# Kernel optimization log

Measured on AMD Instinct MI355X. Metric: run time of the kernel, lower is better.

## Reference

```python
import jax, jax.numpy as jnp
import numpy as np

B, T, L = 64, 1024, 400
E, D, A, K = 512, 80, 512, 5  # enc_odim, dec_odim, attn_dim, num mixture components


def setup_inputs() -> dict:
    key = jax.random.key(0)
    ks = jax.random.split(key, 24)
    g = lambda k, shape, fan: jax.random.normal(k, shape, jnp.float32) / np.sqrt(fan)
    return {
        "enc_z": jax.random.normal(ks[0], (B, T, E), jnp.float32),
        "ys": jax.random.normal(ks[1], (B, L, D), jnp.float32),
        "pre_W1": g(ks[2], (D, D), D), "pre_b1": jnp.zeros((D,), jnp.float32),
        "pre_W2": g(ks[3], (D, D), D), "pre_b2": jnp.zeros((D,), jnp.float32),
        # MOL attention GRU cell: input D -> hidden A (gates r,z,n)
        "gru_Wx": g(ks[4], (D, 3 * A), D), "gru_Wh": g(ks[5], (A, 3 * A), A),
        "gru_bx": jnp.zeros((3 * A,), jnp.float32), "gru_bh": jnp.zeros((3 * A,), jnp.float32),
        # MOL param net: Linear(A,A) + tanh + Linear(A, 3K)
        "att_W1": g(ks[6], (A, A), A), "att_b1": jnp.zeros((A,), jnp.float32),
        "att_W2": g(ks[7], (A, 3 * K), A), "att_b2": jnp.zeros((3 * K,), jnp.float32),
        # 2-layer LSTM: layer1 input E+A -> D, layer2 D -> D (gates i,f,g,o)
        "lstm_Wx1": g(ks[8], (E + A, 4 * D), E + A), "lstm_Wh1": g(ks[9], (D, 4 * D), D),
        "lstm_b1": jnp.zeros((4 * D,), jnp.float32),
        "lstm_Wx2": g(ks[10], (D, 4 * D), D), "lstm_Wh2": g(ks[11], (D, 4 * D), D),
        "lstm_b2": jnp.zeros((4 * D,), jnp.float32),
        # stop token projection
        "stop_W": g(ks[12], (D, 1), D), "stop_b": jnp.zeros((1,), jnp.float32),
    }


def _gru_cell(x, h, Wx, Wh, bx, bh):
    gx = x @ Wx + bx
    gh = h @ Wh + bh
    xr, xz, xn = jnp.split(gx, 3, axis=-1)
    hr, hz, hn = jnp.split(gh, 3, axis=-1)
    r = jax.nn.sigmoid(xr + hr)
    z = jax.nn.sigmoid(xz + hz)
    n = jnp.tanh(xn + r * hn)
    return (1.0 - z) * n + z * h


def _lstm_cell(x, h, c, Wx, Wh, b):
    gates = x @ Wx + h @ Wh + b
    i, f, g_, o = jnp.split(gates, 4, axis=-1)
    c_new = jax.nn.sigmoid(f) * c + jax.nn.sigmoid(i) * jnp.tanh(g_)
    h_new = jax.nn.sigmoid(o) * jnp.tanh(c_new)
    return h_new, c_new


def reference(enc_z, ys, pre_W1, pre_b1, pre_W2, pre_b2,
              gru_Wx, gru_Wh, gru_bx, gru_bh,
              att_W1, att_b1, att_W2, att_b2,
              lstm_Wx1, lstm_Wh1, lstm_b1, lstm_Wx2, lstm_Wh2, lstm_b2,
              stop_W, stop_b):
    b, t, e = enc_z.shape
    n_steps = ys.shape[1]
    d = pre_W1.shape[0]
    a = gru_Wh.shape[0]
    k = att_W2.shape[1] // 3
    pos = jnp.arange(t, dtype=jnp.float32)  # encoder positions

    def step(carry, _):
        h_att, means, h1, c1, h2, c2, prev_out = carry
        # prenet (eval mode)
        p = jax.nn.relu(prev_out @ pre_W1 + pre_b1)
        p = jax.nn.relu(p @ pre_W2 + pre_b2)
        # MOL attention: update attention RNN state, predict mixture params
        h_att = _gru_cell(p, h_att, gru_Wx, gru_Wh, gru_bx, gru_bh)
        params = jnp.tanh(h_att @ att_W1 + att_b1) @ att_W2 + att_b2  # [B, 3K]
        mu_hat, s_hat, w_hat = jnp.split(params, 3, axis=-1)
        means = means + jax.nn.softplus(mu_hat)            # monotonic means [B, K]
        scales = jax.nn.softplus(s_hat) + 1e-4             # [B, K]
        mix_w = jax.nn.softmax(w_hat, axis=-1)             # [B, K]
        # attention weights via logistic CDF differences: [B, T, K] -> [B, T]
        z_hi = (pos[None, :, None] + 0.5 - means[:, None, :]) / scales[:, None, :]
        z_lo = (pos[None, :, None] - 0.5 - means[:, None, :]) / scales[:, None, :]
        attn_w = jnp.einsum('btk,bk->bt', jax.nn.sigmoid(z_hi) - jax.nn.sigmoid(z_lo), mix_w)
        context = jnp.einsum('bt,bte->be', attn_w, enc_z)  # [B, E]
        # 2-layer LSTM
        x = jnp.concatenate([context, h_att], axis=-1)     # [B, E+A]
        h1, c1 = _lstm_cell(x, h1, c1, lstm_Wx1, lstm_Wh1, lstm_b1)
        h2, c2 = _lstm_cell(h1, h2, c2, lstm_Wx2, lstm_Wh2, lstm_b2)
        logit = (h2 @ stop_W + stop_b)[:, 0]               # [B]
        new_carry = (h_att, means, h1, c1, h2, c2, h2)     # feedback = decoder output
        return new_carry, (h2, logit)

    zf = lambda *s: jnp.zeros(s, jnp.float32)
    carry0 = (zf(b, a), zf(b, k), zf(b, d), zf(b, d), zf(b, d), zf(b, d), zf(b, d))
    _, (outs, logits) = jax.lax.scan(step, carry0, xs=None, length=n_steps)
    before = jnp.transpose(outs, (1, 0, 2))   # [B, L, D]
    after = before                             # postnet not applied inside loop
    return after, before, jnp.transpose(logits, (1, 0))  # [B, L]
```

## Files before the change

### kernel.cpp

```cpp
#include <hip/hip_runtime.h>

#define NB 256
#define BT 512
#define BB 64
#define TT 1024
#define LL 400
#define EE 512
#define DD 80
#define AA 512
#define KK 5

#define WF_HB 2048
#define WF_PP 34816
#define WF_PL 51200
#define WF_EW 112640
#define WF_EWSZ (64UL*1024UL*320UL)

struct Pr {
  const float *enc;
  const float *pW1,*pb1,*pW2,*pb2;
  const float *gWx,*gWh,*gbx,*gbh;
  const float *aW1,*ab1,*aW2,*ab2;
  const float *lWx1,*lWh1,*lb1,*lWx2,*lWh2,*lb2;
  const float *sW,*sb;
  float *oa,*obf,*ol;
  unsigned *ctr;
  float *hb,*pp,*pls,*ew;
  int useEW;
};

__device__ __forceinline__ float sigm(float x){ return 1.f/(1.f+expf(-x)); }
__device__ __forceinline__ float softplusf(float x){ return fmaxf(x,0.f)+log1pf(expf(-fabsf(x))); }
__device__ __forceinline__ void gstore(float* p, float v){
  __hip_atomic_store(p, v, __ATOMIC_RELAXED, __HIP_MEMORY_SCOPE_AGENT);
}
__device__ __forceinline__ float gload(const float* p){
  return __hip_atomic_load(p, __ATOMIC_RELAXED, __HIP_MEMORY_SCOPE_AGENT);
}
__device__ __forceinline__ void gadd(float* p, float v){
  __hip_atomic_fetch_add(p, v, __ATOMIC_RELAXED, __HIP_MEMORY_SCOPE_AGENT);
}
__device__ __forceinline__ void acc4(float4& a, float w, const float4 x){
  a.x = fmaf(w,x.x,a.x); a.y = fmaf(w,x.y,a.y);
  a.z = fmaf(w,x.z,a.z); a.w = fmaf(w,x.w,a.w);
}

__device__ __forceinline__ void cbar_arrive(unsigned* ctr){
  __syncthreads();
  if (threadIdx.x == 0){
    asm volatile("s_waitcnt vmcnt(0)" ::: "memory");
    __hip_atomic_fetch_add(ctr, 1u, __ATOMIC_RELAXED, __HIP_MEMORY_SCOPE_AGENT);
  }
}
__device__ __forceinline__ void cbar_wait(unsigned* ctr, unsigned& tgt){
  if (threadIdx.x == 0){
    while (__hip_atomic_load(ctr, __ATOMIC_RELAXED, __HIP_MEMORY_SCOPE_AGENT) < tgt)
      __builtin_amdgcn_s_sleep(1);
  }
  __syncthreads();
  tgt += 16;
}

__global__ __launch_bounds__(512) void ew_kernel(const float* __restrict__ enc,
                                                 const float* __restrict__ W,
                                                 float* __restrict__ EW){
  const int b = blockIdx.x, t0 = blockIdx.y*16, tid = threadIdx.x;
  __shared__ float encT[512*16];
  #pragma unroll
  for (int r=0;r<16;++r)
    encT[tid*16+r] = enc[((size_t)b*TT + t0 + r)*EE + tid];
  __syncthreads();
  if (tid < 320){
    float acc[16];
    #pragma unroll
    for (int k=0;k<16;++k) acc[k]=0.f;
    const float* wp = W + tid;
    #pragma unroll 2
    for (int e=0;e<512;++e){
      float w = wp[(size_t)e*320];
      const float4* er = (const float4*)&encT[e*16];
      float4 x0=er[0], x1=er[1], x2=er[2], x3=er[3];
      acc[0]=fmaf(w,x0.x,acc[0]); acc[1]=fmaf(w,x0.y,acc[1]);
      acc[2]=fmaf(w,x0.z,acc[2]); acc[3]=fmaf(w,x0.w,acc[3]);
      acc[4]=fmaf(w,x1.x,acc[4]); acc[5]=fmaf(w,x1.y,acc[5]);
      acc[6]=fmaf(w,x1.z,acc[6]); acc[7]=fmaf(w,x1.w,acc[7]);
      acc[8]=fmaf(w,x2.x,acc[8]); acc[9]=fmaf(w,x2.y,acc[9]);
      acc[10]=fmaf(w,x2.z,acc[10]); acc[11]=fmaf(w,x2.w,acc[11]);
      acc[12]=fmaf(w,x3.x,acc[12]); acc[13]=fmaf(w,x3.y,acc[13]);
      acc[14]=fmaf(w,x3.z,acc[14]); acc[15]=fmaf(w,x3.w,acc[15]);
    }
    #pragma unroll
    for (int k=0;k<16;++k)
      EW[((size_t)b*TT + t0 + k)*320 + tid] = acc[k];
  }
}

__global__ __launch_bounds__(BT) void decoder_kernel(Pr P){
  const int blk = blockIdx.x, tid = threadIdx.x;
  const int sq = blk & 15, coh = blk >> 4;
  const int b0 = coh * 4;
  unsigned* ctr = P.ctr + coh*64;

  __shared__ float4 hj4[512];
  __shared__ float4 pj4[DD];
  __shared__ float4 h1j4[DD];
  __shared__ float4 h2j4[DD];
  __shared__ float4 qs4[32];
  __shared__ float4 ctx4[32];
  __shared__ float4 l2a4[320];
  __shared__ float4 scr4[2048];
  __shared__ float  awb[4][1024];
  __shared__ float  c1s[4][80], c2s[4][80];
  __shared__ float  pv[4][16], msta[4][8], mscl[4][8], mwt[4][8];
  __shared__ float  stp[320];
  __shared__ int    wlo[4], whi[4];

  float* hjF=(float*)hj4;  float* pjF=(float*)pj4;  float* h1F=(float*)h1j4;
  float* h2F=(float*)h2j4; float* scrF=(float*)scr4; float* qsF=(float*)qs4;

  { float4 z{};
    for (int i=tid;i<512;i+=BT) hj4[i]=z;
    for (int i=tid;i<1536;i+=BT) scr4[512+i]=z;
    if (tid<DD){ h1j4[tid]=z; h2j4[tid]=z; }
    if (tid<320){ c1s[tid&3][tid>>2]=0.f; c2s[tid&3][tid>>2]=0.f; }
    if (tid<32) msta[tid>>3][tid&7]=0.f;
  }
  if (tid<320){
    #pragma unroll
    for (int par=0;par<3;++par)
      #pragma unroll
      for (int g=0;g<4;++g)
        gstore(&P.pls[par*20480 + (size_t)(b0+g)*320 + tid], 0.f);
  }
  unsigned tgt = 16;
  cbar_arrive(ctr); cbar_wait(ctr, tgt);

  for (int l=0; l<LL; ++l){
    float* plA = P.pls + (l%3)*20480;
    float* plZ = P.pls + ((l+1)%3)*20480;

    if (tid<320){
      const int col=tid>>2, g=tid&3;
      float s=P.pb1[col];
      #pragma unroll 4
      for (int j=0;j<DD;++j) s = fmaf(h2F[j*4+g], P.pW1[j*DD+col], s);
      scrF[col*4+g]=fmaxf(s,0.f);
    }
    __syncthreads();
    if (tid<320){
      const int col=tid>>2, g=tid&3;
      float s=P.pb2[col];
      #pragma unroll 4
      for (int j=0;j<DD;++j) s = fmaf(scrF[j*4+g], P.pW2[j*DD+col], s);
      pjF[col*4+g]=fmaxf(s,0.f);
    }
    __syncthreads();

    if (tid<128){
      const int u = tid & 31, psl = tid >> 5;
      const int cb = sq*32 + u;
      float4 ar{}, az{}, axn{};
      const int j0 = psl*20;
      #pragma unroll 4
      for (int jj=0;jj<20;++jj){
        const int j = j0+jj;
        float4 x = pj4[j];
        const float* W = P.gWx + (size_t)j*1536 + cb;
        acc4(ar,W[0],x); acc4(az,W[512],x); acc4(axn,W[1024],x);
      }
      scr4[0*128 + psl*32+u]=ar;
      scr4[1*128 + psl*32+u]=az;
      scr4[2*128 + psl*32+u]=axn;
    }
    __syncthreads();
    if (tid<128){
      const int u=tid>>2, g=tid&3, uu=sq*32+u;
      float rx=0,zx=0,xn=0,hn=0;
      #pragma unroll
      for (int k=0;k<4;++k){
        rx += scrF[(0*128+k*32+u)*4+g];
        zx += scrF[(1*128+k*32+u)*4+g];
        xn += scrF[(2*128+k*32+u)*4+g];
      }
      #pragma unroll
      for (int k=0;k<16;++k){
        rx += scrF[(512 + 0*512 + k*32+u)*4+g];
        zx += scrF[(512 + 1*512 + k*32+u)*4+g];
        hn += scrF[(512 + 2*512 + k*32+u)*4+g];
      }
      float r = sigm(rx + P.gbx[uu] + P.gbh[uu]);
      float z = sigm(zx + P.gbx[512+uu] + P.gbh[512+uu]);
      float n = tanhf(xn + P.gbx[1024+uu] + r*(hn + P.gbh[1024+uu]));
      float ho = (1.f-z)*n + z*hjF[uu*4+g];
      gstore(&P.hb[(size_t)(b0+g)*512 + uu], ho);
    }
    cbar_arrive(ctr);
    if (tid<320){
      float4 a{};
      const float* W = P.lWh2 + tid;
      #pragma unroll 4
      for (int j=0;j<DD;++j) acc4(a, W[(size_t)j*320], h2j4[j]);
      l2a4[tid]=a;
    }
    cbar_wait(ctr, tgt);
    {
      float4 h;
      h.x=gload(&P.hb[(size_t)(b0+0)*512+tid]);
      h.y=gload(&P.hb[(size_t)(b0+1)*512+tid]);
      h.z=gload(&P.hb[(size_t)(b0+2)*512+tid]);
      h.w=gload(&P.hb[(size_t)(b0+3)*512+tid]);
      hj4[tid]=h;
    }
    __syncthreads();

    {
      const int c = tid & 31, jsl = tid >> 5, j0 = jsl*32;
      float4 a{};
      const float* W = P.aW1 + (size_t)j0*512 + sq*32 + c;
      #pragma unroll 4
      for (int jj=0;jj<32;++jj) acc4(a, W[(size_t)jj*512], hj4[j0+jj]);
      scr4[jsl*32+c]=a;
    }
    __syncthreads();
    if (tid<128){
      const int c=tid>>2, g=tid&3;
      float s=0.f;
      #pragma unroll
      for (int k=0;k<16;++k) s += scrF[(k*32+c)*4+g];
      qsF[c*4+g] = tanhf(s + P.ab1[sq*32+c]);
    }
    __syncthreads();
    if (tid<60){
      const int col=tid%15, g=tid/15;
      float s=0.f;
      #pragma unroll 4
      for (int j=0;j<32;++j) s = fmaf(qsF[j*4+g], P.aW2[(size_t)(sq*32+j)*15+col], s);
      gstore(&P.pp[(size_t)(b0+g)*256 + sq*16 + col], s);
    }
    cbar_arrive(ctr);
    float4 l1acc{};
    if (tid<320){
      { const float* W = P.lWx1 + (size_t)(512+sq*32)*320 + tid;
        #pragma unroll 4
        for (int j=0;j<32;++j) acc4(l1acc, W[(size_t)j*320], hj4[sq*32+j]); }
      { const float* W = P.lWh1 + (size_t)(sq*5)*320 + tid;
        #pragma unroll
        for (int j=0;j<5;++j)  acc4(l1acc, W[(size_t)j*320], h1j4[sq*5+j]); }
    }
    cbar_wait(ctr, tgt);
    if (tid<60){
      const int col=tid%15, g=tid/15;
      float s=P.ab2[col];
      #pragma unroll
      for (int k=0;k<16;++k) s += gload(&P.pp[(size_t)(b0+g)*256 + k*16 + col]);
      pv[g][col]=s;
    }
    __syncthreads();
    if (tid<4){
      const int g=tid;
      float lo=3.4e38f, hi=-3.4e38f, mmax=-3.4e38f;
      #pragma unroll
      for (int k=0;k<KK;++k){
        float m = msta[g][k] + softplusf(pv[g][k]);
        msta[g][k]=m;
        float sc = softplusf(pv[g][5+k]) + 1e-4f;
        mscl[g][k]=sc;
        mmax = fmaxf(mmax, pv[g][10+k]);
        lo = fminf(lo, m-0.5f-26.f*sc);
        hi = fmaxf(hi, m+0.5f+26.f*sc);
      }
      float den=0.f;
      #pragma unroll
      for (int k=0;k<KK;++k){ float e=expf(pv[g][10+k]-mmax); mwt[g][k]=e; den+=e; }
      float rd=1.f/den;
      #pragma unroll
      for (int k=0;k<KK;++k) mwt[g][k]*=rd;
      int ilo=(int)fmaxf(0.f,floorf(lo));
      int ihi=(int)fminf((float)TT,ceilf(hi)+1.f);
      if (ihi<ilo) ihi=ilo;
      wlo[g]=ilo; whi[g]=ihi;
    }
    __syncthreads();

    if (P.useEW){
      { const int g = tid>>7, lane = tid&127;
        const int lo_=wlo[g], hi_=whi[g];
        for (int t = lo_+lane; t < hi_; t += 128){
          const float tf=(float)t;
          float s=0.f;
          #pragma unroll
          for (int k=0;k<KK;++k){
            float mu=msta[g][k], sc=mscl[g][k];
            s += mwt[g][k]*(sigm((tf+0.5f-mu)/sc)-sigm((tf-0.5f-mu)/sc));
          }
          awb[g][t-lo_]=s;
        }
      }
      __syncthreads();
      if (tid<320){
        float* lp=(float*)&l1acc;
        const float* EWb = P.ew;
        #pragma unroll
        for (int g=0;g<4;++g){
          const int lo_=wlo[g], hi_=whi[g];
          for (int t=lo_+sq; t<hi_; t+=16)
            lp[g] = fmaf(awb[g][t-lo_], EWb[((size_t)(b0+g)*TT+t)*320+tid], lp[g]);
        }
      }
    } else {
      { const int eq = tid&7, g = (tid>>3)&3, ts = tid>>5;
        const float* bz = P.enc + (size_t)(b0+g)*TT*EE + sq*32 + eq*4;
        float4 acc{};
        for (int t = wlo[g]+ts; t < whi[g]; t += 16){
          const float tf=(float)t;
          float awv=0.f;
          #pragma unroll
          for (int k=0;k<KK;++k){
            float mu=msta[g][k], sc=mscl[g][k];
            awv += mwt[g][k]*(sigm((tf+0.5f-mu)/sc)-sigm((tf-0.5f-mu)/sc));
          }
          float4 v = *(const float4*)(bz+(size_t)t*EE);
          acc.x=fmaf(awv,v.x,acc.x); acc.y=fmaf(awv,v.y,acc.y);
          acc.z=fmaf(awv,v.z,acc.z); acc.w=fmaf(awv,v.w,acc.w);
        }
        ((float4*)scrF)[ts*32 + g*8 + eq]=acc;
      }
      __syncthreads();
      if (tid<128){
        const int g=tid>>5, e=tid&31;
        float s=0.f;
        #pragma unroll
        for (int k=0;k<16;++k) s += scrF[(k*32 + g*8 + (e>>2))*4 + (e&3)];
        ((float*)&ctx4[e])[g]=s;
      }
      __syncthreads();
      if (tid<320){
        const float* W = P.lWx1 + (size_t)(sq*32)*320 + tid;
        #pragma unroll 4
        for (int j=0;j<32;++j) acc4(l1acc, W[(size_t)j*320], ctx4[j]);
      }
    }
    if (tid<320){
      float* lp=(float*)&l1acc;
      #pragma unroll
      for (int g=0;g<4;++g) gadd(&plA[(size_t)(b0+g)*320 + tid], lp[g]);
    }
    cbar_arrive(ctr);
    {
      const int u = tid & 31, hsl = tid >> 5;
      const int cb = sq*32 + u;
      float4 ar{}, az{}, ahn{};
      const int h0 = hsl*32;
      #pragma unroll 4
      for (int jj=0;jj<32;++jj){
        float4 x = hj4[h0+jj];
        const float* W = P.gWh + (size_t)(h0+jj)*1536 + cb;
        acc4(ar,W[0],x); acc4(az,W[512],x); acc4(ahn,W[1024],x);
      }
      scr4[512 + 0*512 + hsl*32+u]=ar;
      scr4[512 + 1*512 + hsl*32+u]=az;
      scr4[512 + 2*512 + hsl*32+u]=ahn;
    }
    cbar_wait(ctr, tgt);
    if (tid<320){
      const int u=tid>>2, g=tid&3;
      float gate[4];
      #pragma unroll
      for (int gg=0;gg<4;++gg)
        gate[gg] = gload(&plA[(size_t)(b0+g)*320 + gg*80 + u]) + P.lb1[gg*80+u];
      float i_=sigm(gate[0]), f_=sigm(gate[1]), g_=tanhf(gate[2]), o_=sigm(gate[3]);
      float cn=f_*c1s[g][u]+i_*g_;
      c1s[g][u]=cn;
      h1F[u*4+g]=o_*tanhf(cn);
    }
    if (sq==0 && tid<320){
      #pragma unroll
      for (int g=0;g<4;++g) gstore(&plZ[(size_t)(b0+g)*320 + tid], 0.f);
    }
    __syncthreads();
    if (tid<320){
      float4 a = l2a4[tid];
      const float* W = P.lWx2 + tid;
      #pragma unroll 4
      for (int j=0;j<DD;++j) acc4(a, W[(size_t)j*320], h1j4[j]);
      const float bb=P.lb2[tid];
      a.x+=bb; a.y+=bb; a.z+=bb; a.w+=bb;
      scr4[tid]=a;
    }
    __syncthreads();
    if (tid<320){
      const int u=tid>>2, g=tid&3;
      float i_=sigm(scrF[(0*80+u)*4+g]);
      float f_=sigm(scrF[(1*80+u)*4+g]);
      float g_=tanhf(scrF[(2*80+u)*4+g]);
      float o_=sigm(scrF[(3*80+u)*4+g]);
      float cn=f_*c2s[g][u]+i_*g_;
      c2s[g][u]=cn;
      float hn=o_*tanhf(cn);
      h2F[u*4+g]=hn;
      stp[u*4+g]=hn*P.sW[u];
      if (sq==0){
        const size_t o=((size_t)(b0+g)*LL+l)*DD+u;
        P.oa[o]=hn; P.obf[o]=hn;
      }
    }
    __syncthreads();
    if (tid<4 && sq==0){
      float s=P.sb[0];
      for (int u=0;u<DD;++u) s+=stp[u*4+tid];
      P.ol[(size_t)(b0+tid)*LL+l]=s;
    }
  }
}

extern "C" void kernel_launch(void* const* d_in, const int* in_sizes, int n_in,
                              void* d_out, int out_size, void* d_ws, size_t ws_size,
                              hipStream_t stream){
  (void)in_sizes; (void)n_in; (void)out_size;
  if (ws_size < (size_t)WF_EW*sizeof(float)) return;
  const int useEW = ws_size >= (size_t)(WF_EW + WF_EWSZ)*sizeof(float);

  hipMemsetAsync(d_ws, 0, 8192, stream);

  Pr P;
  P.enc = (const float*)d_in[0];
  P.pW1=(const float*)d_in[2];  P.pb1=(const float*)d_in[3];
  P.pW2=(const float*)d_in[4];  P.pb2=(const float*)d_in[5];
  P.gWx=(const float*)d_in[6];  P.gWh=(const float*)d_in[7];
  P.gbx=(const float*)d_in[8];  P.gbh=(const float*)d_in[9];
  P.aW1=(const float*)d_in[10]; P.ab1=(const float*)d_in[11];
  P.aW2=(const float*)d_in[12]; P.ab2=(const float*)d_in[13];
  P.lWx1=(const float*)d_in[14]; P.lWh1=(const float*)d_in[15]; P.lb1=(const float*)d_in[16];
  P.lWx2=(const float*)d_in[17]; P.lWh2=(const float*)d_in[18]; P.lb2=(const float*)d_in[19];
  P.sW=(const float*)d_in[20];  P.sb=(const float*)d_in[21];

  float* ws = (float*)d_ws;
  P.ctr = (unsigned*)ws;
  P.hb  = ws + WF_HB;
  P.pp  = ws + WF_PP;
  P.pls = ws + WF_PL;
  P.ew  = ws + WF_EW;
  P.useEW = useEW;

  if (useEW)
    ew_kernel<<<dim3(BB, TT/16), 512, 0, stream>>>(P.enc, P.lWx1, P.ew);

  float* o = (float*)d_out;
  P.oa  = o;
  P.obf = o + (size_t)BB*LL*DD;
  P.ol  = o + (size_t)2*BB*LL*DD;

  void* args[] = { (void*)&P };
  hipLaunchCooperativeKernel((void*)decoder_kernel, dim3(NB), dim3(BT), args, 0, stream);
}
```

Measured before the change: 11.26 ms.

## Overlap barrier waits with prefetch, tighten attention window, spread output writes

Moves the LSTM layer-1 recurrent partial product into an earlier barrier-wait slot. That slot now also prefetches the upcoming encoder-projection window rows into cache, using the previous step's window plus a margin. The attention window half-width shrinks from 26 to 16 scale units, which cuts the number of timesteps processed. Zeroing of the next partial-sum buffer is split across all blocks instead of block 0, and output writes rotate among blocks per step. The narrower window changes the numerics slightly, and the prefetch adds memory traffic that may be wasted.

```diff
diff --git a/kernel.cpp b/kernel.cpp
--- a/kernel.cpp
+++ b/kernel.cpp
@@ -124,6 +124,7 @@
     if (tid<DD){ h1j4[tid]=z; h2j4[tid]=z; }
     if (tid<320){ c1s[tid&3][tid>>2]=0.f; c2s[tid&3][tid>>2]=0.f; }
     if (tid<32) msta[tid>>3][tid&7]=0.f;
+    if (tid<4){ wlo[tid]=0; whi[tid]=0; }
   }
   if (tid<320){
     #pragma unroll
@@ -138,6 +139,7 @@
   for (int l=0; l<LL; ++l){
     float* plA = P.pls + (l%3)*20480;
     float* plZ = P.pls + ((l+1)%3)*20480;
+    const int wr = l & 15;
 
     if (tid<320){
       const int col=tid>>2, g=tid&3;
@@ -194,6 +196,7 @@
       float ho = (1.f-z)*n + z*hjF[uu*4+g];
       gstore(&P.hb[(size_t)(b0+g)*512 + uu], ho);
     }
+    float4 l1acc{};
     cbar_arrive(ctr);
     if (tid<320){
       float4 a{};
@@ -201,6 +204,22 @@
       #pragma unroll 4
       for (int j=0;j<DD;++j) acc4(a, W[(size_t)j*320], h2j4[j]);
       l2a4[tid]=a;
+    }
+    if (tid<320){
+      const float* W = P.lWh1 + (size_t)(sq*5)*320 + tid;
+      #pragma unroll
+      for (int j=0;j<5;++j) acc4(l1acc, W[(size_t)j*320], h1j4[sq*5+j]);
+    }
+    if (P.useEW && tid<320){
+      float pf = 0.f;
+      #pragma unroll
+      for (int g=0;g<4;++g){
+        const int lo_=wlo[g];
+        const int hi_ = (whi[g]+24 < TT) ? whi[g]+24 : TT;
+        for (int t=lo_+sq; t<hi_; t+=16)
+          pf += P.ew[((size_t)(b0+g)*TT+t)*320 + tid];
+      }
+      asm volatile("" :: "v"(pf));
     }
     cbar_wait(ctr, tgt);
     {
@@ -238,14 +257,10 @@
       gstore(&P.pp[(size_t)(b0+g)*256 + sq*16 + col], s);
     }
     cbar_arrive(ctr);
-    float4 l1acc{};
-    if (tid<320){
-      { const float* W = P.lWx1 + (size_t)(512+sq*32)*320 + tid;
-        #pragma unroll 4
-        for (int j=0;j<32;++j) acc4(l1acc, W[(size_t)j*320], hj4[sq*32+j]); }
-      { const float* W = P.lWh1 + (size_t)(sq*5)*320 + tid;
-        #pragma unroll
-        for (int j=0;j<5;++j)  acc4(l1acc, W[(size_t)j*320], h1j4[sq*5+j]); }
+    if (tid<320){
+      const float* W = P.lWx1 + (size_t)(512+sq*32)*320 + tid;
+      #pragma unroll 4
+      for (int j=0;j<32;++j) acc4(l1acc, W[(size_t)j*320], hj4[sq*32+j]);
     }
     cbar_wait(ctr, tgt);
     if (tid<60){
@@ -266,8 +281,8 @@
         float sc = softplusf(pv[g][5+k]) + 1e-4f;
         mscl[g][k]=sc;
         mmax = fmaxf(mmax, pv[g][10+k]);
-        lo = fminf(lo, m-0.5f-26.f*sc);
-        hi = fmaxf(hi, m+0.5f+26.f*sc);
+        lo = fminf(lo, m-0.5f-16.f*sc);
+        hi = fmaxf(hi, m+0.5f+16.f*sc);
       }
       float den=0.f;
       #pragma unroll
@@ -345,6 +360,10 @@
       #pragma unroll
       for (int g=0;g<4;++g) gadd(&plA[(size_t)(b0+g)*320 + tid], lp[g]);
     }
+    if (tid>=384 && tid<464){
+      const int t2=tid-384, c=sq*20+(t2>>2), g=t2&3;
+      gstore(&plZ[(size_t)(b0+g)*320 + c], 0.f);
+    }
     cbar_arrive(ctr);
     {
       const int u = tid & 31, hsl = tid >> 5;
@@ -372,10 +391,6 @@
       float cn=f_*c1s[g][u]+i_*g_;
       c1s[g][u]=cn;
       h1F[u*4+g]=o_*tanhf(cn);
-    }
-    if (sq==0 && tid<320){
-      #pragma unroll
-      for (int g=0;g<4;++g) gstore(&plZ[(size_t)(b0+g)*320 + tid], 0.f);
     }
     __syncthreads();
     if (tid<320){
@@ -399,13 +414,13 @@
       float hn=o_*tanhf(cn);
       h2F[u*4+g]=hn;
       stp[u*4+g]=hn*P.sW[u];
-      if (sq==0){
+      if (sq==wr){
         const size_t o=((size_t)(b0+g)*LL+l)*DD+u;
         P.oa[o]=hn; P.obf[o]=hn;
       }
     }
     __syncthreads();
-    if (tid<4 && sq==0){
+    if (tid<4 && sq==wr){
       float s=P.sb[0];
       for (int u=0;u<DD;++u) s+=stp[u*4+tid];
       P.ol[(size_t)(b0+tid)*LL+l]=s;
```

New measurement: 12.02 ms. 6.8% more time.
